# Optimization experiments

Hardware: AMD Instinct MI355X
Metric: run time of the kernel (lower is better)

## Reference

```python
import jax, jax.numpy as jnp
import numpy as np

H = 8; DH = 32; MAX_HOP = 256; NUM_EDGE = 25
NHOP = MAX_HOP + 2   # 258 (incl. UNREACHABLE)
NEDGE = NUM_EDGE + 2 # 27  (incl. NO_EDGE)


def _ln(x, g, b, eps=1e-5):
    m = x.mean(-1, keepdims=True)
    v = ((x - m) ** 2).mean(-1, keepdims=True)
    return (x - m) / jnp.sqrt(v + eps) * g + b


def _scatter_bins(att, idx, M):
    # att: [B,H,N,N] probs, idx: [B,N,N] int bins -> [B,H,N,M] scatter-add over keys
    B, Hh, N, _ = att.shape
    idxb = jnp.broadcast_to(idx[:, None, :, :], att.shape)
    bi = jnp.arange(B)[:, None, None, None]
    hi = jnp.arange(Hh)[None, :, None, None]
    ni = jnp.arange(N)[None, None, :, None]
    return jnp.zeros((B, Hh, N, M), att.dtype).at[bi, hi, ni, idxb].add(att)


def _forward(x, mask, distance_mat, edge_attr_mat,
             node_W, node_b, ln1_g, ln1_b, Wq, bq, Wk, bk, Wv, bv, Wo, bo,
             ln2_g, ln2_b, W1, b1, W2, b2,
             q_hop, q_edge, k_hop, k_edge, v_hop, v_edge,
             fln_g, fln_b, out_W, out_b):
    B, N, _ = x.shape
    h = x @ node_W + node_b  # [B,N,DM]
    # index preprocessing (clamp then -1 -> sentinel, as in torch)
    dist = jnp.minimum(distance_mat, MAX_HOP)
    dist = jnp.where(dist == -1, MAX_HOP + 1, dist)
    edge = jnp.minimum(edge_attr_mat, NUM_EDGE)
    edge = jnp.where(edge == -1, NUM_EDGE + 1, edge)

    # ---- encoder layer ----
    y = _ln(h, ln1_g, ln1_b)
    q = (y @ Wq + bq).reshape(B, N, H, DH).transpose(0, 2, 1, 3)  # bhnd
    k = (y @ Wk + bk).reshape(B, N, H, DH).transpose(0, 2, 1, 3)
    v = (y @ Wv + bv).reshape(B, N, H, DH).transpose(0, 2, 1, 3)
    Qh = q_hop.reshape(NHOP, H, DH).transpose(1, 0, 2)   # [H,M,d]
    Qe = q_edge.reshape(NEDGE, H, DH).transpose(1, 0, 2)
    Kh = k_hop.reshape(NHOP, H, DH).transpose(1, 0, 2)
    Ke = k_edge.reshape(NEDGE, H, DH).transpose(1, 0, 2)
    Vh = v_hop.reshape(NHOP, H, DH).transpose(1, 0, 2)
    Ve = v_edge.reshape(NEDGE, H, DH).transpose(1, 0, 2)

    dist_b = jnp.broadcast_to(dist[:, None, :, :], (B, H, N, N))
    edge_b = jnp.broadcast_to(edge[:, None, :, :], (B, H, N, N))

    qh = jnp.einsum('bhnd,hmd->bhnm', q, Qh)  # [B,H,N,M]
    query_hop = jnp.take_along_axis(qh, dist_b, axis=3)
    qe = jnp.einsum('bhnd,hmd->bhnm', q, Qe)
    query_edge = jnp.take_along_axis(qe, edge_b, axis=3)
    kh = jnp.einsum('bhnd,hmd->bhnm', k, Kh)
    # torch gathers along dim 2 of kh^T: key_hop[b,h,i,j] = k_j . Kh[dist[i,j]]
    key_hop = jnp.take_along_axis(jnp.swapaxes(kh, 2, 3), dist_b, axis=2)
    ke = jnp.einsum('bhnd,hmd->bhnm', k, Ke)
    key_edge = jnp.take_along_axis(ke, edge_b, axis=3)

    scale = DH ** (-0.5)
    scores = (jnp.einsum('bhid,bhjd->bhij', q, k)
              + (query_hop + key_hop) + (query_edge + key_edge)) * scale
    scores = jnp.where(mask[:, None, None, :], -jnp.inf, scores)
    att = jax.nn.softmax(scores, axis=-1)

    vha = _scatter_bins(att, dist, NHOP)   # [B,H,N,NHOP]
    vea = _scatter_bins(att, edge, NEDGE)
    ctx = (jnp.einsum('bhij,bhjd->bhid', att, v)
           + jnp.einsum('bhim,hmd->bhid', vha, Vh)
           + jnp.einsum('bhim,hmd->bhid', vea, Ve))
    ctx = ctx.transpose(0, 2, 1, 3).reshape(B, N, H * DH)
    h = h + (ctx @ Wo + bo)

    y = _ln(h, ln2_g, ln2_b)
    y = jax.nn.gelu(y @ W1 + b1, approximate=False) @ W2 + b2
    h = h + y
    # ---- head ----
    out = _ln(h, fln_g, fln_b)
    return out @ out_W + out_b


def setup_inputs() -> dict:
    key = jax.random.key(0)
    ks = jax.random.split(key, 40)
    D_IN, DM, FF, OUT, B, N = 128, 256, 1024, 128, 16, 512
    nrm = lambda k, shape, s=0.02: jax.random.normal(k, shape, jnp.float32) * s
    z = lambda shape: jnp.zeros(shape, jnp.float32)
    o = lambda shape: jnp.ones(shape, jnp.float32)
    return {
        'x': jax.random.normal(ks[0], (B, N, D_IN), jnp.float32),
        'mask': jnp.zeros((B, N), bool),
        'distance_mat': jax.random.randint(ks[1], (B, N, N), 0, 257),
        'edge_attr_mat': jax.random.randint(ks[2], (B, N, N), 0, 26),
        'node_W': nrm(ks[3], (D_IN, DM)), 'node_b': z((DM,)),
        'ln1_g': o((DM,)), 'ln1_b': z((DM,)),
        'Wq': nrm(ks[4], (DM, DM)), 'bq': z((DM,)),
        'Wk': nrm(ks[5], (DM, DM)), 'bk': z((DM,)),
        'Wv': nrm(ks[6], (DM, DM)), 'bv': z((DM,)),
        'Wo': nrm(ks[7], (DM, DM)), 'bo': z((DM,)),
        'ln2_g': o((DM,)), 'ln2_b': z((DM,)),
        'W1': nrm(ks[8], (DM, FF)), 'b1': z((FF,)),
        'W2': nrm(ks[9], (FF, DM)), 'b2': z((DM,)),
        'q_hop': nrm(ks[10], (NHOP, DM)), 'q_edge': nrm(ks[11], (NEDGE, DM)),
        'k_hop': nrm(ks[12], (NHOP, DM)), 'k_edge': nrm(ks[13], (NEDGE, DM)),
        'v_hop': nrm(ks[14], (NHOP, DM)), 'v_edge': nrm(ks[15], (NEDGE, DM)),
        'fln_g': o((DM,)), 'fln_b': z((DM,)),
        'out_W': nrm(ks[16], (DM, OUT)), 'out_b': z((OUT,)),
    }


def reference(x, mask, distance_mat, edge_attr_mat,
              node_W, node_b, ln1_g, ln1_b, Wq, bq, Wk, bk, Wv, bv, Wo, bo,
              ln2_g, ln2_b, W1, b1, W2, b2,
              q_hop, q_edge, k_hop, k_edge, v_hop, v_edge,
              fln_g, fln_b, out_W, out_b):
    return _forward(x, mask, distance_mat, edge_attr_mat,
                    node_W, node_b, ln1_g, ln1_b, Wq, bq, Wk, bk, Wv, bv, Wo, bo,
                    ln2_g, ln2_b, W1, b1, W2, b2,
                    q_hop, q_edge, k_hop, k_edge, v_hop, v_edge,
                    fln_g, fln_b, out_W, out_b)
```

## Files before the change

### kernel.cpp

```cpp
#include <hip/hip_runtime.h>
#include <hip/hip_bf16.h>
#include <math.h>

#define BB 16
#define NN 512
#define DIN 128
#define DM 256
#define NH 8
#define DH 32
#define FF 1024
#define DOUT 128
#define NHOP 258
#define NEDGE 27
#define ROWS (BB*NN)
#define QHE_S 296

typedef short short8 __attribute__((ext_vector_type(8)));
typedef float f32x4 __attribute__((ext_vector_type(4)));

static __device__ __forceinline__ float bf2f(unsigned short u) {
    union { float f; unsigned int i; } c; c.i = ((unsigned int)u) << 16; return c.f;
}
static __device__ __forceinline__ short f2bs(float f) {
    __hip_bfloat16 h = __float2bfloat16(f);
    return *reinterpret_cast<short*>(&h);
}

__global__ __launch_bounds__(256) void k_ln(const float* __restrict__ in, const float* __restrict__ g,
                                            const float* __restrict__ bta, float* __restrict__ out) {
    int row = blockIdx.x * 4 + (threadIdx.x >> 6);
    int l = threadIdx.x & 63;
    float4 xv = ((const float4*)(in + (size_t)row*DM))[l];
    float s = xv.x + xv.y + xv.z + xv.w;
    #pragma unroll
    for (int o = 32; o > 0; o >>= 1) s += __shfl_xor(s, o, 64);
    float mean = s * (1.0f/DM);
    float dx = xv.x-mean, dy = xv.y-mean, dz = xv.z-mean, dw = xv.w-mean;
    float vs = dx*dx + dy*dy + dz*dz + dw*dw;
    #pragma unroll
    for (int o = 32; o > 0; o >>= 1) vs += __shfl_xor(vs, o, 64);
    float r = rsqrtf(vs * (1.0f/DM) + 1e-5f);
    float4 gg = ((const float4*)g)[l];
    float4 bb = ((const float4*)bta)[l];
    float4 ov; ov.x = dx*r*gg.x+bb.x; ov.y = dy*r*gg.y+bb.y; ov.z = dz*r*gg.z+bb.z; ov.w = dw*r*gg.w+bb.w;
    ((float4*)(out + (size_t)row*DM))[l] = ov;
}

template<int K, int N, int ACT, int RES, int QKV>
__global__ __launch_bounds__(256) void k_mgemm(const float* __restrict__ A, const float* __restrict__ W,
                                               const float* __restrict__ bias, float* __restrict__ out) {
    __shared__ __align__(16) short As[64][40];
    __shared__ __align__(16) short Bs[64][40];
    int r0 = blockIdx.x * 64;
    int n0 = blockIdx.y * 64;
    int tid = threadIdx.x;
    int w = tid >> 6, l = tid & 63;

    f32x4 acc[4];
    #pragma unroll
    for (int c = 0; c < 4; ++c) acc[c] = (f32x4){0.f,0.f,0.f,0.f};

    for (int k0 = 0; k0 < K; k0 += 32) {
        __syncthreads();
        {
            int m = tid >> 2, ks = (tid & 3) * 8;
            const float* src = A + (size_t)(r0 + m)*K + k0 + ks;
            float4 f0 = *(const float4*)src;
            float4 f1 = *(const float4*)(src + 4);
            short8 pk;
            pk[0]=f2bs(f0.x); pk[1]=f2bs(f0.y); pk[2]=f2bs(f0.z); pk[3]=f2bs(f0.w);
            pk[4]=f2bs(f1.x); pk[5]=f2bs(f1.y); pk[6]=f2bs(f1.z); pk[7]=f2bs(f1.w);
            *(short8*)&As[m][ks] = pk;
        }
        {
            int n = tid & 63, kg = tid >> 6;
            const float* wp = W + (size_t)(k0 + kg*8)*N + n0 + n;
            short8 pk;
            #pragma unroll
            for (int j = 0; j < 8; ++j) pk[j] = f2bs(wp[(size_t)j*N]);
            *(short8*)&Bs[n][kg*8] = pk;
        }
        __syncthreads();
        short8 af = *(short8*)&As[w*16 + (l & 15)][(l >> 4)*8];
        #pragma unroll
        for (int c = 0; c < 4; ++c) {
            short8 bf = *(short8*)&Bs[c*16 + (l & 15)][(l >> 4)*8];
            acc[c] = __builtin_amdgcn_mfma_f32_16x16x32_bf16(af, bf, acc[c], 0, 0, 0);
        }
    }

    int quad = l >> 4;
    #pragma unroll
    for (int c = 0; c < 4; ++c) {
        int col = n0 + c*16 + (l & 15);
        float bv = bias[col];
        #pragma unroll
        for (int reg = 0; reg < 4; ++reg) {
            int row = r0 + w*16 + quad*4 + reg;
            float val = acc[c][reg] + bv;
            if (ACT) val = 0.5f * val * (1.0f + erff(val * 0.70710678118654752f));
            if (QKV) {
                int b = row >> 9, n = row & (NN-1);
                int hh = col >> 5, d = col & (DH-1);
                out[(size_t)((b*NH + hh)*NN + n)*DH + d] = val;
            } else if (RES) {
                out[(size_t)row*N + col] += val;
            } else {
                out[(size_t)row*N + col] = val;
            }
        }
    }
}

__global__ __launch_bounds__(256) void k_trd(const float* __restrict__ in, float* __restrict__ out, int M) {
    int m = blockIdx.x, t = threadIdx.x;
    out[(size_t)t*M + m] = in[(size_t)m*DM + t];
}

__global__ __launch_bounds__(256) void k_vhve(const float* __restrict__ vh, const float* __restrict__ ve,
                                              float* __restrict__ out) {
    int m = blockIdx.x;
    int t = threadIdx.x;
    float val = 0.f;
    if (m < NHOP) val = vh[(size_t)m*DM + t];
    else if (m >= 264 && m < 264 + NEDGE) val = ve[(size_t)(m - 264)*DM + t];
    out[((size_t)(t >> 5)*QHE_S + m)*DH + (t & 31)] = val;
}

__global__ __launch_bounds__(256) void k_tx(const float* __restrict__ k, float* __restrict__ kT) {
    __shared__ float lds[64*33];
    int bh = blockIdx.x;
    int j0 = blockIdx.y * 64;
    int tid = threadIdx.x;
    {
        int jj = tid >> 2, d8 = tid & 3;
        const float* src = k + ((size_t)bh*NN + j0 + jj)*DH + d8*8;
        float4 a = *(const float4*)(src);
        float4 b = *(const float4*)(src + 4);
        float* dst = lds + jj*33 + d8*8;
        dst[0]=a.x; dst[1]=a.y; dst[2]=a.z; dst[3]=a.w;
        dst[4]=b.x; dst[5]=b.y; dst[6]=b.z; dst[7]=b.w;
    }
    __syncthreads();
    {
        int d = tid >> 3, jg = tid & 7;
        float* dst = kT + ((size_t)bh*DH + d)*NN + j0;
        #pragma unroll
        for (int jj2 = 0; jj2 < 8; ++jj2) {
            int j = jg*8 + jj2;
            dst[j] = lds[j*33 + d];
        }
    }
}

__global__ __launch_bounds__(256) void k_kht(const float* __restrict__ kT, const float* __restrict__ k_hop,
                                             __hip_bfloat16* __restrict__ kht) {
    int bm = blockIdx.x;
    int m = bm % NHOP;
    int bh = bm / NHOP;
    int hh = bh & (NH-1);
    float kh[32];
    {
        const float4* khp = (const float4*)(k_hop + (size_t)m*DM + hh*DH);
        #pragma unroll
        for (int c = 0; c < 8; ++c) *(float4*)&kh[c*4] = khp[c];
    }
    const float* kTb = kT + (size_t)bh*DH*NN;
    #pragma unroll
    for (int it = 0; it < 2; ++it) {
        int j = threadIdx.x + it*256;
        float acc = 0.f;
        #pragma unroll
        for (int d = 0; d < DH; ++d) acc += kh[d] * kTb[(size_t)d*NN + j];
        kht[(size_t)bm*NN + j] = __float2bfloat16(acc);
    }
}

__global__ __launch_bounds__(256) void k_qhe(const float* __restrict__ q, const float* __restrict__ k,
                                             const float* __restrict__ Qh_d, const float* __restrict__ Qe_d,
                                             const float* __restrict__ Ke_d, unsigned short* __restrict__ qhe) {
    int bh = blockIdx.x;
    int hh = bh & (NH-1);
    int i0 = blockIdx.y * 16;
    int tid = threadIdx.x;
    __shared__ __align__(16) float As[16][32];
    __shared__ __align__(16) float Ks[16][32];
    {
        int r = (tid & 127) >> 3, c4 = tid & 7;
        const float* src = ((tid < 128) ? q : k) + ((size_t)bh*NN + i0 + r)*DH + c4*4;
        float4 vv = *(const float4*)src;
        float* dst = (tid < 128) ? &As[r][c4*4] : &Ks[r][c4*4];
        *(float4*)dst = vv;
    }
    __syncthreads();
    {
        float acc[16];
        #pragma unroll
        for (int r = 0; r < 16; ++r) acc[r] = 0.f;
        const float* wb = Qh_d + (size_t)hh*32*NHOP + tid;
        for (int d = 0; d < 32; ++d) {
            float wv = wb[(size_t)d*NHOP];
            #pragma unroll
            for (int r = 0; r < 16; ++r) acc[r] += As[r][d] * wv;
        }
        #pragma unroll
        for (int r = 0; r < 16; ++r)
            qhe[((size_t)bh*NN + i0 + r)*QHE_S + tid] = (unsigned short)f2bs(acc[r]);
    }
    if (tid < 2) {
        int m = 256 + tid;
        float acc[16];
        #pragma unroll
        for (int r = 0; r < 16; ++r) acc[r] = 0.f;
        const float* wb = Qh_d + (size_t)hh*32*NHOP + m;
        for (int d = 0; d < 32; ++d) {
            float wv = wb[(size_t)d*NHOP];
            #pragma unroll
            for (int r = 0; r < 16; ++r) acc[r] += As[r][d] * wv;
        }
        #pragma unroll
        for (int r = 0; r < 16; ++r)
            qhe[((size_t)bh*NN + i0 + r)*QHE_S + m] = (unsigned short)f2bs(acc[r]);
    } else if (tid >= 8 && tid < 8 + NEDGE) {
        int e = tid - 8;
        float acc[16];
        #pragma unroll
        for (int r = 0; r < 16; ++r) acc[r] = 0.f;
        const float* wq = Qe_d + (size_t)hh*32*NEDGE + e;
        const float* wk = Ke_d + (size_t)hh*32*NEDGE + e;
        for (int d = 0; d < 32; ++d) {
            float a = wq[(size_t)d*NEDGE], bbw = wk[(size_t)d*NEDGE];
            #pragma unroll
            for (int r = 0; r < 16; ++r) acc[r] += As[r][d]*a + Ks[r][d]*bbw;
        }
        #pragma unroll
        for (int r = 0; r < 16; ++r)
            qhe[((size_t)bh*NN + i0 + r)*QHE_S + 264 + e] = (unsigned short)f2bs(acc[r]);
    }
}

__global__ __launch_bounds__(256) void k_score(
    const float* __restrict__ q, const float* __restrict__ kT, const float* __restrict__ v,
    const __hip_bfloat16* __restrict__ kht, const int* __restrict__ dist, const int* __restrict__ edge,
    const unsigned char* __restrict__ mask, unsigned short* __restrict__ qhe,
    float* __restrict__ ctx)
{
    int g   = blockIdx.x;
    int r   = g >> 3;
    int b   = (g & 7) + ((r >> 8) << 3);
    int rem = r & 255;
    int i0  = (rem >> 1) * 4;
    int hg  = rem & 1;
    int w   = threadIdx.x >> 6;
    int l   = threadIdx.x & 63;
    int hh  = hg*4 + w;
    int bh  = b*NH + hh;

    __shared__ unsigned short mje[4][NN];
    __shared__ float qv[4][4][DH];
    __shared__ __hip_bfloat16 pb[4][4][NN];
    __shared__ float bins[4][292];

    {
        int t = threadIdx.x;
        int row = t >> 6, c0 = t & 63;
        #pragma unroll
        for (int rep = 0; rep < 2; ++rep) {
            int c4 = c0 + rep*64;
            int4 dv = ((const int4*)(dist + ((size_t)(b*NN) + i0 + row)*NN))[c4];
            int4 ev = ((const int4*)(edge + ((size_t)(b*NN) + i0 + row)*NN))[c4];
            int m0 = dv.x > 256 ? 256 : dv.x; if (dv.x < 0) m0 = 257;
            int m1 = dv.y > 256 ? 256 : dv.y; if (dv.y < 0) m1 = 257;
            int m2 = dv.z > 256 ? 256 : dv.z; if (dv.z < 0) m2 = 257;
            int m3 = dv.w > 256 ? 256 : dv.w; if (dv.w < 0) m3 = 257;
            int e0 = ev.x > 25 ? 25 : ev.x; if (ev.x < 0) e0 = 26;
            int e1 = ev.y > 25 ? 25 : ev.y; if (ev.y < 0) e1 = 26;
            int e2 = ev.z > 25 ? 25 : ev.z; if (ev.z < 0) e2 = 26;
            int e3 = ev.w > 25 ? 25 : ev.w; if (ev.w < 0) e3 = 26;
            mje[row][c4*4+0] = (unsigned short)(m0 | (e0 << 9));
            mje[row][c4*4+1] = (unsigned short)(m1 | (e1 << 9));
            mje[row][c4*4+2] = (unsigned short)(m2 | (e2 << 9));
            mje[row][c4*4+3] = (unsigned short)(m3 | (e3 << 9));
        }
        #pragma unroll
        for (int rep = 0; rep < 2; ++rep) {
            int i = rep*2 + (l >> 5), d = l & 31;
            qv[w][i][d] = q[((size_t)bh*NN + i0 + i)*DH + d];
        }
        for (int s = l; s < 292; s += 64) bins[w][s] = 0.f;
    }
    __syncthreads();

    float sc[4][8];
    #pragma unroll
    for (int i = 0; i < 4; ++i)
        #pragma unroll
        for (int s = 0; s < 8; ++s) sc[i][s] = 0.f;
    {
        const float* kTb = kT + (size_t)bh*DH*NN;
        for (int d = 0; d < 32; ++d) {
            const float* kr = kTb + (size_t)d*NN + l;
            float k0 = kr[0],   k1 = kr[64],  k2 = kr[128], k3 = kr[192];
            float k4 = kr[256], k5 = kr[320], k6 = kr[384], k7 = kr[448];
            float qa = qv[w][0][d], qb = qv[w][1][d], qc = qv[w][2][d], qd = qv[w][3][d];
            sc[0][0]+=qa*k0; sc[0][1]+=qa*k1; sc[0][2]+=qa*k2; sc[0][3]+=qa*k3;
            sc[0][4]+=qa*k4; sc[0][5]+=qa*k5; sc[0][6]+=qa*k6; sc[0][7]+=qa*k7;
            sc[1][0]+=qb*k0; sc[1][1]+=qb*k1; sc[1][2]+=qb*k2; sc[1][3]+=qb*k3;
            sc[1][4]+=qb*k4; sc[1][5]+=qb*k5; sc[1][6]+=qb*k6; sc[1][7]+=qb*k7;
            sc[2][0]+=qc*k0; sc[2][1]+=qc*k1; sc[2][2]+=qc*k2; sc[2][3]+=qc*k3;
            sc[2][4]+=qc*k4; sc[2][5]+=qc*k5; sc[2][6]+=qc*k6; sc[2][7]+=qc*k7;
            sc[3][0]+=qd*k0; sc[3][1]+=qd*k1; sc[3][2]+=qd*k2; sc[3][3]+=qd*k3;
            sc[3][4]+=qd*k4; sc[3][5]+=qd*k5; sc[3][6]+=qd*k6; sc[3][7]+=qd*k7;
        }
    }

    const __hip_bfloat16* khtb = kht + (size_t)bh*NHOP*NN;
    const unsigned char* mrow = mask + (size_t)b*NN;
    unsigned char msk[8];
    #pragma unroll
    for (int s = 0; s < 8; ++s) msk[s] = mrow[l + 64*s];
    const float scale = 0.17677669529663687f;

    #pragma unroll
    for (int i = 0; i < 4; ++i) {
        unsigned short* qhr = qhe + ((size_t)bh*NN + i0 + i)*QHE_S;
        int pk[8];
        #pragma unroll
        for (int s = 0; s < 8; ++s) pk[s] = mje[i][l + 64*s];
        unsigned short raw[8];
        #pragma unroll
        for (int s = 0; s < 8; ++s)
            raw[s] = ((const unsigned short*)khtb)[(size_t)(pk[s] & 511)*NN + l + 64*s];
        unsigned short qhv[8], qev[8];
        #pragma unroll
        for (int s = 0; s < 8; ++s) qhv[s] = qhr[pk[s] & 511];
        #pragma unroll
        for (int s = 0; s < 8; ++s) qev[s] = qhr[264 + (pk[s] >> 9)];
        float x[8];
        #pragma unroll
        for (int s = 0; s < 8; ++s) {
            float a = (sc[i][s] + bf2f(qhv[s]) + bf2f(raw[s]) + bf2f(qev[s])) * scale;
            if (msk[s]) a = -INFINITY;
            x[s] = a;
        }
        float mx = x[0];
        #pragma unroll
        for (int s = 1; s < 8; ++s) mx = fmaxf(mx, x[s]);
        #pragma unroll
        for (int o = 32; o > 0; o >>= 1) mx = fmaxf(mx, __shfl_xor(mx, o, 64));
        float sum = 0.f;
        #pragma unroll
        for (int s = 0; s < 8; ++s) { x[s] = __expf(x[s] - mx); sum += x[s]; }
        #pragma unroll
        for (int o = 32; o > 0; o >>= 1) sum += __shfl_xor(sum, o, 64);
        float inv = 1.0f / sum;
        #pragma unroll
        for (int s = 0; s < 8; ++s) {
            float ps = x[s] * inv;
            pb[w][i][l + 64*s] = __float2bfloat16(ps);
            atomicAdd(&bins[w][pk[s] & 511], ps);
            atomicAdd(&bins[w][264 + (pk[s] >> 9)], ps);
        }
        #pragma unroll
        for (int s5 = 0; s5 < 5; ++s5) {
            int idx = l + 64*s5;
            if (idx < 292) {
                qhr[idx] = (unsigned short)f2bs(bins[w][idx]);
                if (i < 3) bins[w][idx] = 0.f;
            }
        }
    }

    int jc = l >> 3, d4 = l & 7;
    float4 acc[4];
    #pragma unroll
    for (int i = 0; i < 4; ++i) { acc[i].x = acc[i].y = acc[i].z = acc[i].w = 0.f; }
    {
        const float* vb = v + (size_t)bh*NN*DH + d4*4;
        for (int off = 0; off < 64; ++off) {
            int j = 8*off + jc;
            float4 vv = *(const float4*)(vb + (size_t)j*DH);
            #pragma unroll
            for (int i = 0; i < 4; ++i) {
                float p = bf2f(*(const unsigned short*)&pb[w][i][j]);
                acc[i].x += p*vv.x; acc[i].y += p*vv.y; acc[i].z += p*vv.z; acc[i].w += p*vv.w;
            }
        }
    }
    #pragma unroll
    for (int i = 0; i < 4; ++i) {
        #pragma unroll
        for (int o = 8; o <= 32; o <<= 1) {
            acc[i].x += __shfl_xor(acc[i].x, o, 64);
            acc[i].y += __shfl_xor(acc[i].y, o, 64);
            acc[i].z += __shfl_xor(acc[i].z, o, 64);
            acc[i].w += __shfl_xor(acc[i].w, o, 64);
        }
        if (jc == 0) {
            *(float4*)(ctx + ((size_t)b*NN + i0 + i)*DM + hh*DH + d4*4) = acc[i];
        }
    }
}

__global__ __launch_bounds__(512) void k_av(const unsigned short* __restrict__ vha,
                                            const float* __restrict__ vhve, float* __restrict__ ctx) {
    int bh = blockIdx.x;
    int hh = bh & (NH-1);
    int b  = bh >> 3;
    int i0 = blockIdx.y * 16;
    __shared__ unsigned short lds[16*QHE_S];
    int tid = threadIdx.x;
    for (int idx = tid; idx < 16*QHE_S; idx += 512) {
        int rr = idx / QHE_S, c = idx - rr*QHE_S;
        lds[idx] = vha[((size_t)bh*NN + i0 + rr)*QHE_S + c];
    }
    __syncthreads();
    int i = tid >> 5, d = tid & 31;
    const float* tb = vhve + (size_t)hh*QHE_S*DH + d;
    const unsigned short* pr = &lds[i*QHE_S];
    float acc = 0.f;
    #pragma unroll 4
    for (int m = 0; m < 292; ++m) {
        acc += bf2f(pr[m]) * tb[(size_t)m*DH];
    }
    ctx[((size_t)b*NN + i0 + i)*DM + hh*DH + d] += acc;
}

extern "C" void kernel_launch(void* const* d_in, const int* in_sizes, int n_in,
                              void* d_out, int out_size, void* d_ws, size_t ws_size,
                              hipStream_t stream) {
    const float* x     = (const float*)d_in[0];
    const unsigned char* mask = (const unsigned char*)d_in[1];
    const int*   dist  = (const int*)d_in[2];
    const int*   edge  = (const int*)d_in[3];
    const float* node_W = (const float*)d_in[4];
    const float* node_b = (const float*)d_in[5];
    const float* ln1_g = (const float*)d_in[6];
    const float* ln1_b = (const float*)d_in[7];
    const float* Wq = (const float*)d_in[8];
    const float* bq = (const float*)d_in[9];
    const float* Wk = (const float*)d_in[10];
    const float* bk = (const float*)d_in[11];
    const float* Wv = (const float*)d_in[12];
    const float* bv = (const float*)d_in[13];
    const float* Wo = (const float*)d_in[14];
    const float* bo = (const float*)d_in[15];
    const float* ln2_g = (const float*)d_in[16];
    const float* ln2_b = (const float*)d_in[17];
    const float* W1 = (const float*)d_in[18];
    const float* b1 = (const float*)d_in[19];
    const float* W2 = (const float*)d_in[20];
    const float* b2 = (const float*)d_in[21];
    const float* q_hop  = (const float*)d_in[22];
    const float* q_edge = (const float*)d_in[23];
    const float* k_hop  = (const float*)d_in[24];
    const float* k_edge = (const float*)d_in[25];
    const float* v_hop  = (const float*)d_in[26];
    const float* v_edge = (const float*)d_in[27];
    const float* fln_g = (const float*)d_in[28];
    const float* fln_b = (const float*)d_in[29];
    const float* out_W = (const float*)d_in[30];
    const float* out_b = (const float*)d_in[31];
    float* out = (float*)d_out;

    float* ws = (float*)d_ws;
    float* h   = ws + 0;
    float* y   = ws + 2097152;
    float* q   = ws + 4194304;
    float* k   = ws + 6291456;
    float* v   = ws + 8388608;
    float* ctx = ws + 10485760;
    __hip_bfloat16* kht = (__hip_bfloat16*)(ws + 12582912);
    float* ffn = ws + 12582912;
    float* kT  = ws + 21037056;
    unsigned short* qhe = (unsigned short*)(ws + 23134208);
    float* Qh_d = y + 0;
    float* Qe_d = y + 66048;
    float* Ke_d = y + 72960;
    float* vhve = y + 81920;

    k_mgemm<DIN, DM, 0, 0, 0><<<dim3(ROWS/64, DM/64), 256, 0, stream>>>(x, node_W, node_b, h);
    k_ln<<<ROWS/4, 256, 0, stream>>>(h, ln1_g, ln1_b, y);
    k_mgemm<DM, DM, 0, 0, 1><<<dim3(ROWS/64, DM/64), 256, 0, stream>>>(y, Wq, bq, q);
    k_mgemm<DM, DM, 0, 0, 1><<<dim3(ROWS/64, DM/64), 256, 0, stream>>>(y, Wk, bk, k);
    k_mgemm<DM, DM, 0, 0, 1><<<dim3(ROWS/64, DM/64), 256, 0, stream>>>(y, Wv, bv, v);
    k_trd<<<NHOP, 256, 0, stream>>>(q_hop, Qh_d, NHOP);
    k_trd<<<NEDGE, 256, 0, stream>>>(q_edge, Qe_d, NEDGE);
    k_trd<<<NEDGE, 256, 0, stream>>>(k_edge, Ke_d, NEDGE);
    k_vhve<<<QHE_S, 256, 0, stream>>>(v_hop, v_edge, vhve);
    k_tx<<<dim3(BB*NH, 8), 256, 0, stream>>>(k, kT);
    k_kht<<<BB*NH*NHOP, 256, 0, stream>>>(kT, k_hop, kht);
    k_qhe<<<dim3(BB*NH, NN/16), 256, 0, stream>>>(q, k, Qh_d, Qe_d, Ke_d, qhe);
    k_score<<<BB*(NN/4)*2, 256, 0, stream>>>(q, kT, v, kht, dist, edge, mask, qhe, ctx);
    k_av<<<dim3(BB*NH, NN/16), 512, 0, stream>>>(qhe, vhve, ctx);
    k_mgemm<DM, DM, 0, 1, 0><<<dim3(ROWS/64, DM/64), 256, 0, stream>>>(ctx, Wo, bo, h);
    k_ln<<<ROWS/4, 256, 0, stream>>>(h, ln2_g, ln2_b, y);
    k_mgemm<DM, FF, 1, 0, 0><<<dim3(ROWS/64, FF/64), 256, 0, stream>>>(y, W1, b1, ffn);
    k_mgemm<FF, DM, 0, 1, 0><<<dim3(ROWS/64, DM/64), 256, 0, stream>>>(ffn, W2, b2, h);
    k_ln<<<ROWS/4, 256, 0, stream>>>(h, fln_g, fln_b, y);
    k_mgemm<DM, DOUT, 0, 0, 0><<<dim3(ROWS/64, DOUT/64), 256, 0, stream>>>(y, out_W, out_b, out);
}
```

Measured before the change: 866.5 us.

## Move hop/edge projection and AV side-products onto bf16 MFMA kernels

Replaces the scalar fp32 kernels for the key-hop projection, the query hop/edge projection and the hop/edge value aggregation with MFMA 16x16x32 bf16 kernels. A single prep kernel now packs the hop/edge weight tables into padded bf16 layouts, replacing four separate transpose launches. The aim is to cut the FMA-bound cost of these side products and the launch overhead. In exchange, the K and q inputs and the weight tables are rounded to bf16. The AV kernel also reads padded columns past each row, which only works because the matching value-table entries are zero.

```diff
diff --git a/kernel.cpp b/kernel.cpp
--- a/kernel.cpp
+++ b/kernel.cpp
@@ -112,19 +112,30 @@
     }
 }
 
-__global__ __launch_bounds__(256) void k_trd(const float* __restrict__ in, float* __restrict__ out, int M) {
-    int m = blockIdx.x, t = threadIdx.x;
-    out[(size_t)t*M + m] = in[(size_t)m*DM + t];
-}
-
-__global__ __launch_bounds__(256) void k_vhve(const float* __restrict__ vh, const float* __restrict__ ve,
-                                              float* __restrict__ out) {
-    int m = blockIdx.x;
-    int t = threadIdx.x;
-    float val = 0.f;
-    if (m < NHOP) val = vh[(size_t)m*DM + t];
-    else if (m >= 264 && m < 264 + NEDGE) val = ve[(size_t)(m - 264)*DM + t];
-    out[((size_t)(t >> 5)*QHE_S + m)*DH + (t & 31)] = val;
+__global__ __launch_bounds__(256) void k_prep(const float* __restrict__ q_hop, const float* __restrict__ q_edge,
+                                              const float* __restrict__ k_edge, const float* __restrict__ v_hop,
+                                              const float* __restrict__ v_edge,
+                                              unsigned short* __restrict__ w2, unsigned short* __restrict__ vhve_d) {
+    int h = blockIdx.x;
+    int tid = threadIdx.x;
+    for (int idx = tid; idx < 304*64; idx += 256) {
+        int n = idx >> 6, kk = idx & 63;
+        float val = 0.f;
+        if (n < NHOP && kk < 32) val = q_hop[(size_t)n*DM + h*DH + kk];
+        else if (n >= 264 && n < 264 + NEDGE) {
+            int e = n - 264;
+            val = (kk < 32) ? q_edge[(size_t)e*DM + h*DH + kk]
+                            : k_edge[(size_t)e*DM + h*DH + (kk - 32)];
+        }
+        w2[((size_t)h*304 + n)*64 + kk] = (unsigned short)f2bs(val);
+    }
+    for (int idx = tid; idx < 32*320; idx += 256) {
+        int d = idx / 320, kk = idx - d*320;
+        float val = 0.f;
+        if (kk < NHOP) val = v_hop[(size_t)kk*DM + h*DH + d];
+        else if (kk >= 264 && kk < 264 + NEDGE) val = v_edge[(size_t)(kk-264)*DM + h*DH + d];
+        vhve_d[((size_t)h*32 + d)*320 + kk] = (unsigned short)f2bs(val);
+    }
 }
 
 __global__ __launch_bounds__(256) void k_tx(const float* __restrict__ k, float* __restrict__ kT) {
@@ -153,89 +164,87 @@
     }
 }
 
-__global__ __launch_bounds__(256) void k_kht(const float* __restrict__ kT, const float* __restrict__ k_hop,
-                                             __hip_bfloat16* __restrict__ kht) {
-    int bm = blockIdx.x;
-    int m = bm % NHOP;
-    int bh = bm / NHOP;
-    int hh = bh & (NH-1);
-    float kh[32];
-    {
-        const float4* khp = (const float4*)(k_hop + (size_t)m*DM + hh*DH);
-        #pragma unroll
-        for (int c = 0; c < 8; ++c) *(float4*)&kh[c*4] = khp[c];
-    }
-    const float* kTb = kT + (size_t)bh*DH*NN;
-    #pragma unroll
-    for (int it = 0; it < 2; ++it) {
-        int j = threadIdx.x + it*256;
-        float acc = 0.f;
-        #pragma unroll
-        for (int d = 0; d < DH; ++d) acc += kh[d] * kTb[(size_t)d*NN + j];
-        kht[(size_t)bm*NN + j] = __float2bfloat16(acc);
-    }
-}
-
-__global__ __launch_bounds__(256) void k_qhe(const float* __restrict__ q, const float* __restrict__ k,
-                                             const float* __restrict__ Qh_d, const float* __restrict__ Qe_d,
-                                             const float* __restrict__ Ke_d, unsigned short* __restrict__ qhe) {
+__global__ __launch_bounds__(256) void k_kht2(const float* __restrict__ k, const float* __restrict__ k_hop,
+                                              __hip_bfloat16* __restrict__ kht) {
+    __shared__ __align__(16) short kb[512][40];
     int bh = blockIdx.x;
     int hh = bh & (NH-1);
-    int i0 = blockIdx.y * 16;
+    int r0 = blockIdx.y * 64;
     int tid = threadIdx.x;
-    __shared__ __align__(16) float As[16][32];
-    __shared__ __align__(16) float Ks[16][32];
-    {
-        int r = (tid & 127) >> 3, c4 = tid & 7;
-        const float* src = ((tid < 128) ? q : k) + ((size_t)bh*NN + i0 + r)*DH + c4*4;
-        float4 vv = *(const float4*)src;
-        float* dst = (tid < 128) ? &As[r][c4*4] : &Ks[r][c4*4];
-        *(float4*)dst = vv;
-    }
+    int w = tid >> 6, l = tid & 63;
+    int quad = l >> 4, lr = l & 15;
+
+    #pragma unroll
+    for (int t = 0; t < 8; ++t) {
+        int idx = tid + t*256;
+        int row = idx >> 2, c = idx & 3;
+        const float* src = k + ((size_t)bh*NN + row)*DH + c*8;
+        float4 f0 = *(const float4*)src;
+        float4 f1 = *(const float4*)(src + 4);
+        short8 pk;
+        pk[0]=f2bs(f0.x); pk[1]=f2bs(f0.y); pk[2]=f2bs(f0.z); pk[3]=f2bs(f0.w);
+        pk[4]=f2bs(f1.x); pk[5]=f2bs(f1.y); pk[6]=f2bs(f1.z); pk[7]=f2bs(f1.w);
+        *(short8*)&kb[row][c*8] = pk;
+    }
+    int m = r0 + w*16 + lr;
+    int mc = m < NHOP ? m : NHOP-1;
+    const float* ar = k_hop + (size_t)mc*DM + hh*DH + quad*8;
+    float4 a0 = *(const float4*)ar;
+    float4 a1 = *(const float4*)(ar + 4);
+    short8 af;
+    af[0]=f2bs(a0.x); af[1]=f2bs(a0.y); af[2]=f2bs(a0.z); af[3]=f2bs(a0.w);
+    af[4]=f2bs(a1.x); af[5]=f2bs(a1.y); af[6]=f2bs(a1.z); af[7]=f2bs(a1.w);
     __syncthreads();
-    {
-        float acc[16];
-        #pragma unroll
-        for (int r = 0; r < 16; ++r) acc[r] = 0.f;
-        const float* wb = Qh_d + (size_t)hh*32*NHOP + tid;
-        for (int d = 0; d < 32; ++d) {
-            float wv = wb[(size_t)d*NHOP];
+
+    for (int ct = 0; ct < 32; ++ct) {
+        short8 bf = *(short8*)&kb[ct*16 + lr][quad*8];
+        f32x4 acc = (f32x4){0.f,0.f,0.f,0.f};
+        acc = __builtin_amdgcn_mfma_f32_16x16x32_bf16(af, bf, acc, 0, 0, 0);
+        #pragma unroll
+        for (int reg = 0; reg < 4; ++reg) {
+            int m2 = r0 + w*16 + quad*4 + reg;
+            if (m2 < NHOP)
+                kht[((size_t)bh*NHOP + m2)*NN + ct*16 + lr] = __float2bfloat16(acc[reg]);
+        }
+    }
+}
+
+__global__ __launch_bounds__(256) void k_qhe2(const float* __restrict__ q, const float* __restrict__ k,
+                                              const unsigned short* __restrict__ w2,
+                                              unsigned short* __restrict__ qhe) {
+    int bh = blockIdx.x;
+    int hh = bh & (NH-1);
+    int r0 = blockIdx.y * 64;
+    int tid = threadIdx.x;
+    int w = tid >> 6, l = tid & 63;
+    int quad = l >> 4, lr = l & 15;
+
+    const float* qr = q + ((size_t)bh*NN + r0 + w*16 + lr)*DH + quad*8;
+    const float* kr = k + ((size_t)bh*NN + r0 + w*16 + lr)*DH + quad*8;
+    float4 f0 = *(const float4*)qr, f1 = *(const float4*)(qr + 4);
+    short8 af0;
+    af0[0]=f2bs(f0.x); af0[1]=f2bs(f0.y); af0[2]=f2bs(f0.z); af0[3]=f2bs(f0.w);
+    af0[4]=f2bs(f1.x); af0[5]=f2bs(f1.y); af0[6]=f2bs(f1.z); af0[7]=f2bs(f1.w);
+    f0 = *(const float4*)kr; f1 = *(const float4*)(kr + 4);
+    short8 af1;
+    af1[0]=f2bs(f0.x); af1[1]=f2bs(f0.y); af1[2]=f2bs(f0.z); af1[3]=f2bs(f0.w);
+    af1[4]=f2bs(f1.x); af1[5]=f2bs(f1.y); af1[6]=f2bs(f1.z); af1[7]=f2bs(f1.w);
+
+    const unsigned short* w2h = w2 + (size_t)hh*304*64;
+    for (int ct = 0; ct < 19; ++ct) {
+        int col = ct*16 + lr;
+        short8 b0 = *(const short8*)(w2h + (size_t)col*64 + quad*8);
+        short8 b1 = *(const short8*)(w2h + (size_t)col*64 + 32 + quad*8);
+        f32x4 acc = (f32x4){0.f,0.f,0.f,0.f};
+        acc = __builtin_amdgcn_mfma_f32_16x16x32_bf16(af0, b0, acc, 0, 0, 0);
+        acc = __builtin_amdgcn_mfma_f32_16x16x32_bf16(af1, b1, acc, 0, 0, 0);
+        if (col < QHE_S) {
             #pragma unroll
-            for (int r = 0; r < 16; ++r) acc[r] += As[r][d] * wv;
-        }
-        #pragma unroll
-        for (int r = 0; r < 16; ++r)
-            qhe[((size_t)bh*NN + i0 + r)*QHE_S + tid] = (unsigned short)f2bs(acc[r]);
-    }
-    if (tid < 2) {
-        int m = 256 + tid;
-        float acc[16];
-        #pragma unroll
-        for (int r = 0; r < 16; ++r) acc[r] = 0.f;
-        const float* wb = Qh_d + (size_t)hh*32*NHOP + m;
-        for (int d = 0; d < 32; ++d) {
-            float wv = wb[(size_t)d*NHOP];
-            #pragma unroll
-            for (int r = 0; r < 16; ++r) acc[r] += As[r][d] * wv;
-        }
-        #pragma unroll
-        for (int r = 0; r < 16; ++r)
-            qhe[((size_t)bh*NN + i0 + r)*QHE_S + m] = (unsigned short)f2bs(acc[r]);
-    } else if (tid >= 8 && tid < 8 + NEDGE) {
-        int e = tid - 8;
-        float acc[16];
-        #pragma unroll
-        for (int r = 0; r < 16; ++r) acc[r] = 0.f;
-        const float* wq = Qe_d + (size_t)hh*32*NEDGE + e;
-        const float* wk = Ke_d + (size_t)hh*32*NEDGE + e;
-        for (int d = 0; d < 32; ++d) {
-            float a = wq[(size_t)d*NEDGE], bbw = wk[(size_t)d*NEDGE];
-            #pragma unroll
-            for (int r = 0; r < 16; ++r) acc[r] += As[r][d]*a + Ks[r][d]*bbw;
-        }
-        #pragma unroll
-        for (int r = 0; r < 16; ++r)
-            qhe[((size_t)bh*NN + i0 + r)*QHE_S + 264 + e] = (unsigned short)f2bs(acc[r]);
+            for (int reg = 0; reg < 4; ++reg) {
+                int row = r0 + w*16 + quad*4 + reg;
+                qhe[((size_t)bh*NN + row)*QHE_S + col] = (unsigned short)f2bs(acc[reg]);
+            }
+        }
     }
 }
 
@@ -402,28 +411,38 @@
     }
 }
 
-__global__ __launch_bounds__(512) void k_av(const unsigned short* __restrict__ vha,
-                                            const float* __restrict__ vhve, float* __restrict__ ctx) {
+__global__ __launch_bounds__(256) void k_av2(const unsigned short* __restrict__ vha,
+                                             const unsigned short* __restrict__ vhve_d,
+                                             float* __restrict__ ctx) {
     int bh = blockIdx.x;
     int hh = bh & (NH-1);
     int b  = bh >> 3;
-    int i0 = blockIdx.y * 16;
-    __shared__ unsigned short lds[16*QHE_S];
+    int r0 = blockIdx.y * 64;
     int tid = threadIdx.x;
-    for (int idx = tid; idx < 16*QHE_S; idx += 512) {
-        int rr = idx / QHE_S, c = idx - rr*QHE_S;
-        lds[idx] = vha[((size_t)bh*NN + i0 + rr)*QHE_S + c];
-    }
-    __syncthreads();
-    int i = tid >> 5, d = tid & 31;
-    const float* tb = vhve + (size_t)hh*QHE_S*DH + d;
-    const unsigned short* pr = &lds[i*QHE_S];
-    float acc = 0.f;
-    #pragma unroll 4
-    for (int m = 0; m < 292; ++m) {
-        acc += bf2f(pr[m]) * tb[(size_t)m*DH];
-    }
-    ctx[((size_t)b*NN + i0 + i)*DM + hh*DH + d] += acc;
+    int w = tid >> 6, l = tid & 63;
+    int quad = l >> 4, lr = l & 15;
+
+    const unsigned short* arow = vha + ((size_t)bh*NN + r0 + w*16 + lr)*QHE_S + quad*8;
+    const unsigned short* br0  = vhve_d + ((size_t)hh*32 + lr)*320 + quad*8;
+    const unsigned short* br1  = vhve_d + ((size_t)hh*32 + 16 + lr)*320 + quad*8;
+
+    f32x4 acc0 = (f32x4){0.f,0.f,0.f,0.f};
+    f32x4 acc1 = (f32x4){0.f,0.f,0.f,0.f};
+    #pragma unroll
+    for (int k0 = 0; k0 < 320; k0 += 32) {
+        short8 af = *(const short8*)(arow + k0);
+        short8 b0 = *(const short8*)(br0 + k0);
+        short8 b1 = *(const short8*)(br1 + k0);
+        acc0 = __builtin_amdgcn_mfma_f32_16x16x32_bf16(af, b0, acc0, 0, 0, 0);
+        acc1 = __builtin_amdgcn_mfma_f32_16x16x32_bf16(af, b1, acc1, 0, 0, 0);
+    }
+    #pragma unroll
+    for (int reg = 0; reg < 4; ++reg) {
+        int row = r0 + w*16 + quad*4 + reg;
+        float* cp = ctx + ((size_t)b*NN + row)*DM + hh*DH;
+        cp[lr]      += acc0[reg];
+        cp[16 + lr] += acc1[reg];
+    }
 }
 
 extern "C" void kernel_launch(void* const* d_in, const int* in_sizes, int n_in,
@@ -474,25 +493,20 @@
     float* ffn = ws + 12582912;
     float* kT  = ws + 21037056;
     unsigned short* qhe = (unsigned short*)(ws + 23134208);
-    float* Qh_d = y + 0;
-    float* Qe_d = y + 66048;
-    float* Ke_d = y + 72960;
-    float* vhve = y + 81920;
+    unsigned short* w2     = (unsigned short*)(y);
+    unsigned short* vhve_d = (unsigned short*)(y + 81920);
 
     k_mgemm<DIN, DM, 0, 0, 0><<<dim3(ROWS/64, DM/64), 256, 0, stream>>>(x, node_W, node_b, h);
     k_ln<<<ROWS/4, 256, 0, stream>>>(h, ln1_g, ln1_b, y);
     k_mgemm<DM, DM, 0, 0, 1><<<dim3(ROWS/64, DM/64), 256, 0, stream>>>(y, Wq, bq, q);
     k_mgemm<DM, DM, 0, 0, 1><<<dim3(ROWS/64, DM/64), 256, 0, stream>>>(y, Wk, bk, k);
     k_mgemm<DM, DM, 0, 0, 1><<<dim3(ROWS/64, DM/64), 256, 0, stream>>>(y, Wv, bv, v);
-    k_trd<<<NHOP, 256, 0, stream>>>(q_hop, Qh_d, NHOP);
-    k_trd<<<NEDGE, 256, 0, stream>>>(q_edge, Qe_d, NEDGE);
-    k_trd<<<NEDGE, 256, 0, stream>>>(k_edge, Ke_d, NEDGE);
-    k_vhve<<<QHE_S, 256, 0, stream>>>(v_hop, v_edge, vhve);
+    k_prep<<<NH, 256, 0, stream>>>(q_hop, q_edge, k_edge, v_hop, v_edge, w2, vhve_d);
     k_tx<<<dim3(BB*NH, 8), 256, 0, stream>>>(k, kT);
-    k_kht<<<BB*NH*NHOP, 256, 0, stream>>>(kT, k_hop, kht);
-    k_qhe<<<dim3(BB*NH, NN/16), 256, 0, stream>>>(q, k, Qh_d, Qe_d, Ke_d, qhe);
+    k_kht2<<<dim3(BB*NH, 5), 256, 0, stream>>>(k, k_hop, kht);
+    k_qhe2<<<dim3(BB*NH, NN/64), 256, 0, stream>>>(q, k, w2, qhe);
     k_score<<<BB*(NN/4)*2, 256, 0, stream>>>(q, kT, v, kht, dist, edge, mask, qhe, ctx);
-    k_av<<<dim3(BB*NH, NN/16), 512, 0, stream>>>(qhe, vhve, ctx);
+    k_av2<<<dim3(BB*NH, NN/64), 256, 0, stream>>>(qhe, vhve_d, ctx);
     k_mgemm<DM, DM, 0, 1, 0><<<dim3(ROWS/64, DM/64), 256, 0, stream>>>(ctx, Wo, bo, h);
     k_ln<<<ROWS/4, 256, 0, stream>>>(h, ln2_g, ln2_b, y);
     k_mgemm<DM, FF, 1, 0, 0><<<dim3(ROWS/64, FF/64), 256, 0, stream>>>(y, W1, b1, ffn);
```

Result: faster. 739.5 us (-14.7%).
